# Kernel tuning notes

Hardware: AMD Instinct MI355X
Metric: run time of the kernel (lower is better)

The kernel has to match this reference:

```python
import math
import jax, jax.numpy as jnp
import numpy as np

B, N, D, O, S = 16, 4096, 64, 12, 32
K_TOD, K_DOW = 8, 4
M = K_TOD + K_DOW
A = 32  # attn_dim
ALPHA = 0.1
GATE_BOUND = 1.0
TEMP = 1.0


def setup_inputs() -> dict:
    key = jax.random.key(0)
    ks = jax.random.split(key, 10)
    sc = 0.05
    return {
        "H": jax.random.normal(ks[0], (B, N, D), jnp.float32),
        "ts_out": jax.random.uniform(ks[1], (B, O, 2), jnp.float32),
        "step_emb": jax.random.normal(ks[2], (B, O, S), jnp.float32),
        "key_emb": jax.random.normal(ks[3], (M, A), jnp.float32) * sc,
        "val_emb": jax.random.normal(ks[4], (M, D), jnp.float32) * sc,
        "Wk": jax.random.normal(ks[5], (A, 2), jnp.float32) * sc,
        "Wg": jax.random.normal(ks[6], (1, 2), jnp.float32) * sc,
        "bg": jnp.zeros((1,), jnp.float32),
        "Wq": jax.random.normal(ks[7], (A, D + S), jnp.float32) * sc,
        "bq": jnp.zeros((A,), jnp.float32),
    }


def _fourier_tokens(phase, K):
    # phase: [B,O]; returns [B,O,K,2] of (sin, cos) for harmonics k=1..K
    k = jnp.arange(1, K + 1, dtype=phase.dtype)  # [K]
    ang = 2.0 * math.pi * phase[..., None] * k   # [B,O,K]
    return jnp.stack([jnp.sin(ang), jnp.cos(ang)], axis=-1)


def reference(H, ts_out, step_emb, key_emb, val_emb, Wk, Wg, bg, Wq, bq):
    tod = ts_out[..., 0]
    dow = ts_out[..., 1]
    # Fourier time tokens: [B,O,M,2]
    tok = jnp.concatenate(
        [_fourier_tokens(tod, K_TOD), _fourier_tokens(dow, K_DOW)], axis=2
    )
    # keys / gates / values over the M tokens (tiny side)
    key = jnp.einsum("bomt,at->boma", tok, Wk) + key_emb[None, None]      # [B,O,M,A]
    gate = jnp.tanh(jnp.einsum("bomt,gt->bomg", tok, Wg) + bg) * GATE_BOUND  # [B,O,M,1]
    val = gate * val_emb[None, None]                                       # [B,O,M,D]
    # query: split Linear(D+S) into H-part and step-part to avoid materializing q_in
    qh = jnp.einsum("bnd,ad->bna", H, Wq[:, :D])            # [B,N,A]
    qs = jnp.einsum("bos,as->boa", step_emb, Wq[:, D:]) + bq  # [B,O,A]
    q = qh[:, None, :, :] + qs[:, :, None, :]                # [B,O,N,A]
    scale = 1.0 / (math.sqrt(float(A)) * max(TEMP, 1e-6))
    logits = jnp.einsum("bona,boma->bonm", q, key) * scale   # [B,O,N,M]
    attn = jax.nn.softmax(logits, axis=-1)
    delta = jnp.einsum("bonm,bomd->bond", attn, val)         # [B,O,N,D]
    H_time = H[:, None, :, :] + ALPHA * delta                # [B,O,N,D]
    return (H_time, attn, gate[..., 0])
```

## Files before the change

### kernel.cpp

```cpp
#include <hip/hip_runtime.h>
#include <math.h>

#define BB 16
#define NN 4096
#define DD 64
#define OO 12
#define SS 32
#define MM 12
#define AA 32

__global__ __launch_bounds__(256, 4) void stta_kernel(
    const float* __restrict__ H, const float* __restrict__ ts_out,
    const float* __restrict__ step_emb, const float* __restrict__ key_emb,
    const float* __restrict__ val_emb, const float* __restrict__ Wk,
    const float* __restrict__ Wg, const float* __restrict__ bgp,
    const float* __restrict__ Wq, const float* __restrict__ bq,
    float* __restrict__ out)
{
    const int b = blockIdx.y;
    const int n0 = blockIdx.x * 64;
    const int tid = threadIdx.x;

    __shared__ __align__(16) float s_wq[32 * 64];
    __shared__ __align__(16) float s_ke[MM * AA];
    __shared__ __align__(16) float s_ve[MM * DD];
    __shared__ __align__(16) float s_wk0[32];
    __shared__ __align__(16) float s_wk1[32];
    __shared__ __align__(16) float s_tokS[OO * MM];
    __shared__ __align__(16) float s_tokC[OO * MM];
    __shared__ __align__(16) float s_gate[OO * MM];
    __shared__ __align__(16) float s_qs[OO * AA];
    __shared__ __align__(16) float s_c2[OO * MM];

    float* outH    = out;
    float* outAttn = out + (size_t)BB * OO * NN * DD;
    float* outGate = outAttn + (size_t)BB * OO * NN * MM;

    const float scale = 0.17677669529663687f;

    {
        float4* dst = reinterpret_cast<float4*>(s_wq);
        for (int i = tid; i < 512; i += 256) {
            int a = i >> 4, dq = i & 15;
            dst[i] = reinterpret_cast<const float4*>(Wq + a * 96)[dq];
        }
    }
    {
        float4* dst = reinterpret_cast<float4*>(s_ke);
        const float4* src = reinterpret_cast<const float4*>(key_emb);
        for (int i = tid; i < (MM * AA) / 4; i += 256) dst[i] = src[i];
    }
    {
        float4* dst = reinterpret_cast<float4*>(s_ve);
        const float4* src = reinterpret_cast<const float4*>(val_emb);
        for (int i = tid; i < (MM * DD) / 4; i += 256) dst[i] = src[i];
    }
    if (tid < 32) { s_wk0[tid] = Wk[tid * 2]; s_wk1[tid] = Wk[tid * 2 + 1]; }

    const float wg0 = Wg[0], wg1 = Wg[1], bg0 = bgp[0];
    for (int i = tid; i < OO * MM; i += 256) {
        int o = i / MM, m = i - o * MM;
        float phase = ts_out[(b * OO + o) * 2 + (m < 8 ? 0 : 1)];
        float k = (m < 8) ? (float)(m + 1) : (float)(m - 7);
        float ang = 6.283185307179586f * phase * k;
        float sv = sinf(ang), cv = cosf(ang);
        s_tokS[i] = sv; s_tokC[i] = cv;
        float gv = tanhf(sv * wg0 + cv * wg1 + bg0);
        s_gate[i] = gv;
        if (blockIdx.x == 0) outGate[(b * OO + o) * MM + m] = gv;
    }
    for (int e = tid; e < OO * AA; e += 256) {
        int o = e >> 5, a = e & 31;
        float acc = bq[a];
        const float* se = step_emb + (b * OO + o) * SS;
        const float* wq = Wq + a * 96 + 64;
        #pragma unroll
        for (int s = 0; s < SS; s++) acc += se[s] * wq[s];
        s_qs[e] = acc;
    }
    __syncthreads();

    for (int i = tid; i < OO * MM; i += 256) {
        int o = i / MM, m = i - o * MM;
        float S = s_tokS[i], C = s_tokC[i];
        float acc = 0.f;
        const float* qs = s_qs + o * 32;
        const float* ke = s_ke + m * 32;
        #pragma unroll
        for (int a = 0; a < 32; a++)
            acc += qs[a] * (S * s_wk0[a] + C * s_wk1[a] + ke[a]);
        s_c2[i] = acc * scale;
    }
    __syncthreads();

    const int nl = tid >> 2, g = tid & 3;
    const int n = n0 + nl;

    const float4* hrow = reinterpret_cast<const float4*>(H + ((size_t)b * NN + n) * DD);
    float h[16];
    #pragma unroll
    for (int jj = 0; jj < 4; jj++) {
        float4 v = hrow[g + 4 * jj];
        h[jj*4+0] = v.x; h[jj*4+1] = v.y; h[jj*4+2] = v.z; h[jj*4+3] = v.w;
    }

    float uh = 0.f, vh = 0.f;
    float wh[12] = {0,0,0,0,0,0,0,0,0,0,0,0};
    {
        float qh[32];
        #pragma unroll
        for (int a = 0; a < 32; a++) {
            const float4* wq4 = reinterpret_cast<const float4*>(s_wq + a * 64);
            float acc = 0.f;
            #pragma unroll
            for (int jj = 0; jj < 4; jj++) {
                float4 w = wq4[g + 4 * jj];
                acc += h[jj*4+0]*w.x + h[jj*4+1]*w.y + h[jj*4+2]*w.z + h[jj*4+3]*w.w;
            }
            qh[a] = acc;
        }
        #pragma unroll
        for (int a = 0; a < 32; a++) qh[a] += __shfl_xor(qh[a], 1);
        #pragma unroll
        for (int a = 0; a < 32; a++) qh[a] += __shfl_xor(qh[a], 2);

        const float4* k0 = reinterpret_cast<const float4*>(s_wk0);
        const float4* k1 = reinterpret_cast<const float4*>(s_wk1);
        #pragma unroll
        for (int q = 0; q < 8; q++) {
            float4 a0 = k0[q], a1 = k1[q];
            uh += qh[q*4+0]*a0.x + qh[q*4+1]*a0.y + qh[q*4+2]*a0.z + qh[q*4+3]*a0.w;
            vh += qh[q*4+0]*a1.x + qh[q*4+1]*a1.y + qh[q*4+2]*a1.z + qh[q*4+3]*a1.w;
        }
        #pragma unroll
        for (int m = 0; m < 12; m++) {
            const float4* ke = reinterpret_cast<const float4*>(s_ke + m * 32);
            float acc = 0.f;
            #pragma unroll
            for (int q = 0; q < 8; q++) {
                float4 k4 = ke[q];
                acc += qh[q*4+0]*k4.x + qh[q*4+1]*k4.y + qh[q*4+2]*k4.z + qh[q*4+3]*k4.w;
            }
            wh[m] = acc * scale;
        }
        uh *= scale; vh *= scale;
    }

    const float4* ve4 = reinterpret_cast<const float4*>(s_ve);

    for (int op = 0; op < OO; op += 2) {
        const float4* tS  = reinterpret_cast<const float4*>(s_tokS + op * 12);
        const float4* tC  = reinterpret_cast<const float4*>(s_tokC + op * 12);
        const float4* tc2 = reinterpret_cast<const float4*>(s_c2   + op * 12);
        const float4* tgt = reinterpret_cast<const float4*>(s_gate + op * 12);

        float lg0[12], lg1[12];
        #pragma unroll
        for (int q = 0; q < 3; q++) {
            float4 S = tS[q], C = tC[q], c = tc2[q];
            lg0[q*4+0] = S.x*uh + C.x*vh + wh[q*4+0] + c.x;
            lg0[q*4+1] = S.y*uh + C.y*vh + wh[q*4+1] + c.y;
            lg0[q*4+2] = S.z*uh + C.z*vh + wh[q*4+2] + c.z;
            lg0[q*4+3] = S.w*uh + C.w*vh + wh[q*4+3] + c.w;
        }
        #pragma unroll
        for (int q = 0; q < 3; q++) {
            float4 S = tS[3+q], C = tC[3+q], c = tc2[3+q];
            lg1[q*4+0] = S.x*uh + C.x*vh + wh[q*4+0] + c.x;
            lg1[q*4+1] = S.y*uh + C.y*vh + wh[q*4+1] + c.y;
            lg1[q*4+2] = S.z*uh + C.z*vh + wh[q*4+2] + c.z;
            lg1[q*4+3] = S.w*uh + C.w*vh + wh[q*4+3] + c.w;
        }

        float mx0 = -1e30f, mx1 = -1e30f;
        #pragma unroll
        for (int m = 0; m < 12; m++) { mx0 = fmaxf(mx0, lg0[m]); mx1 = fmaxf(mx1, lg1[m]); }
        float sum0 = 0.f, sum1 = 0.f;
        #pragma unroll
        for (int m = 0; m < 12; m++) {
            lg0[m] = __expf(lg0[m] - mx0); sum0 += lg0[m];
            lg1[m] = __expf(lg1[m] - mx1); sum1 += lg1[m];
        }
        float inv0 = 1.f / sum0, inv1 = 1.f / sum1;
        #pragma unroll
        for (int m = 0; m < 12; m++) { lg0[m] *= inv0; lg1[m] *= inv1; }

        size_t abase0 = ((size_t)(b * OO + op) * NN + n) * MM;
        size_t abase1 = abase0 + (size_t)NN * MM;
        if (g == 0) {
            *reinterpret_cast<float4*>(outAttn + abase0) =
                make_float4(lg0[0], lg0[1], lg0[2], lg0[3]);
            *reinterpret_cast<float4*>(outAttn + abase1) =
                make_float4(lg1[0], lg1[1], lg1[2], lg1[3]);
        } else if (g == 1) {
            *reinterpret_cast<float4*>(outAttn + abase0 + 4) =
                make_float4(lg0[4], lg0[5], lg0[6], lg0[7]);
            *reinterpret_cast<float4*>(outAttn + abase1 + 4) =
                make_float4(lg1[4], lg1[5], lg1[6], lg1[7]);
        } else if (g == 2) {
            *reinterpret_cast<float4*>(outAttn + abase0 + 8) =
                make_float4(lg0[8], lg0[9], lg0[10], lg0[11]);
            *reinterpret_cast<float4*>(outAttn + abase1 + 8) =
                make_float4(lg1[8], lg1[9], lg1[10], lg1[11]);
        }

        #pragma unroll
        for (int q = 0; q < 3; q++) {
            float4 g0 = tgt[q], g1 = tgt[3+q];
            lg0[q*4+0] *= g0.x; lg0[q*4+1] *= g0.y; lg0[q*4+2] *= g0.z; lg0[q*4+3] *= g0.w;
            lg1[q*4+0] *= g1.x; lg1[q*4+1] *= g1.y; lg1[q*4+2] *= g1.z; lg1[q*4+3] *= g1.w;
        }

        size_t hbase = ((size_t)(b * OO + op) * NN + n) * DD;
        float4* outp0 = reinterpret_cast<float4*>(outH + hbase);
        float4* outp1 = reinterpret_cast<float4*>(outH + hbase + (size_t)NN * DD);
        #pragma unroll
        for (int jj = 0; jj < 4; jj++) {
            float ax0=0.f, ay0=0.f, az0=0.f, aw0=0.f;
            float ax1=0.f, ay1=0.f, az1=0.f, aw1=0.f;
            #pragma unroll
            for (int m = 0; m < 12; m++) {
                float4 vv = ve4[m * 16 + g + 4 * jj];
                ax0 += lg0[m]*vv.x; ay0 += lg0[m]*vv.y;
                az0 += lg0[m]*vv.z; aw0 += lg0[m]*vv.w;
                ax1 += lg1[m]*vv.x; ay1 += lg1[m]*vv.y;
                az1 += lg1[m]*vv.z; aw1 += lg1[m]*vv.w;
            }
            outp0[g + 4*jj] = make_float4(h[jj*4+0] + 0.1f*ax0, h[jj*4+1] + 0.1f*ay0,
                                          h[jj*4+2] + 0.1f*az0, h[jj*4+3] + 0.1f*aw0);
            outp1[g + 4*jj] = make_float4(h[jj*4+0] + 0.1f*ax1, h[jj*4+1] + 0.1f*ay1,
                                          h[jj*4+2] + 0.1f*az1, h[jj*4+3] + 0.1f*aw1);
        }
    }
}

extern "C" void kernel_launch(void* const* d_in, const int* in_sizes, int n_in,
                              void* d_out, int out_size, void* d_ws, size_t ws_size,
                              hipStream_t stream) {
    const float* H        = (const float*)d_in[0];
    const float* ts_out   = (const float*)d_in[1];
    const float* step_emb = (const float*)d_in[2];
    const float* key_emb  = (const float*)d_in[3];
    const float* val_emb  = (const float*)d_in[4];
    const float* Wk       = (const float*)d_in[5];
    const float* Wg       = (const float*)d_in[6];
    const float* bg       = (const float*)d_in[7];
    const float* Wq       = (const float*)d_in[8];
    const float* bq       = (const float*)d_in[9];
    float* outp = (float*)d_out;

    dim3 grid(NN / 64, BB);
    stta_kernel<<<grid, 256, 0, stream>>>(H, ts_out, step_emb, key_emb, val_emb,
                                          Wk, Wg, bg, Wq, bq, outp);
}
```

Baseline: 272.3 us.

## Fold Wq into key projections and process two rows per thread

Each block now precomputes a 14x64 matrix that folds Wq together with key_emb and Wk, so each row's logit terms come straight from H with 14 dot products instead of building a 32-wide query and then projecting it. Each thread also handles two rows (128 rows per block, half the grid), which spreads the block setup over more work and reuses the shared-memory loads. This raises register pressure, so launch bounds drop to 2 blocks per SM. The kernel is dominated by output writes, so the compute savings may matter little.

```diff
diff --git a/kernel.cpp b/kernel.cpp
--- a/kernel.cpp
+++ b/kernel.cpp
@@ -9,7 +9,29 @@
 #define MM 12
 #define AA 32
 
-__global__ __launch_bounds__(256, 4) void stta_kernel(
+__device__ __forceinline__ void softmax12(float* lg) {
+    float mx = -1e30f;
+    #pragma unroll
+    for (int m = 0; m < 12; m++) mx = fmaxf(mx, lg[m]);
+    float s = 0.f;
+    #pragma unroll
+    for (int m = 0; m < 12; m++) { lg[m] = __expf(lg[m] - mx); s += lg[m]; }
+    float inv = 1.f / s;
+    #pragma unroll
+    for (int m = 0; m < 12; m++) lg[m] *= inv;
+}
+
+__device__ __forceinline__ void attn_store(float* dst, const float* lg, int g) {
+    if (g == 0) {
+        *reinterpret_cast<float4*>(dst) = make_float4(lg[0], lg[1], lg[2], lg[3]);
+    } else if (g == 1) {
+        *reinterpret_cast<float4*>(dst + 4) = make_float4(lg[4], lg[5], lg[6], lg[7]);
+    } else if (g == 2) {
+        *reinterpret_cast<float4*>(dst + 8) = make_float4(lg[8], lg[9], lg[10], lg[11]);
+    }
+}
+
+__global__ __launch_bounds__(256, 2) void stta_kernel(
     const float* __restrict__ H, const float* __restrict__ ts_out,
     const float* __restrict__ step_emb, const float* __restrict__ key_emb,
     const float* __restrict__ val_emb, const float* __restrict__ Wk,
@@ -18,7 +40,7 @@
     float* __restrict__ out)
 {
     const int b = blockIdx.y;
-    const int n0 = blockIdx.x * 64;
+    const int n0 = blockIdx.x * 128;
     const int tid = threadIdx.x;
 
     __shared__ __align__(16) float s_wq[32 * 64];
@@ -31,6 +53,7 @@
     __shared__ __align__(16) float s_gate[OO * MM];
     __shared__ __align__(16) float s_qs[OO * AA];
     __shared__ __align__(16) float s_c2[OO * MM];
+    __shared__ __align__(16) float s_pm[14 * 64];
 
     float* outH    = out;
     float* outAttn = out + (size_t)BB * OO * NN * DD;
@@ -91,145 +114,135 @@
             acc += qs[a] * (S * s_wk0[a] + C * s_wk1[a] + ke[a]);
         s_c2[i] = acc * scale;
     }
+    for (int i = tid; i < 14 * 64; i += 256) {
+        int j = i >> 6, d = i & 63;
+        const float* coef = (j < 12) ? (s_ke + j * 32) : ((j == 12) ? s_wk0 : s_wk1);
+        float acc = 0.f;
+        #pragma unroll
+        for (int a = 0; a < 32; a++) acc += coef[a] * s_wq[a * 64 + d];
+        s_pm[i] = acc * scale;
+    }
     __syncthreads();
 
     const int nl = tid >> 2, g = tid & 3;
-    const int n = n0 + nl;
-
-    const float4* hrow = reinterpret_cast<const float4*>(H + ((size_t)b * NN + n) * DD);
-    float h[16];
+    const int r0 = n0 + nl;
+    const int r1 = r0 + 64;
+
+    const float4* hA = reinterpret_cast<const float4*>(H + ((size_t)b * NN + r0) * DD);
+    const float4* hB = reinterpret_cast<const float4*>(H + ((size_t)b * NN + r1) * DD);
+    float h0[16], h1[16];
     #pragma unroll
     for (int jj = 0; jj < 4; jj++) {
-        float4 v = hrow[g + 4 * jj];
-        h[jj*4+0] = v.x; h[jj*4+1] = v.y; h[jj*4+2] = v.z; h[jj*4+3] = v.w;
-    }
-
-    float uh = 0.f, vh = 0.f;
-    float wh[12] = {0,0,0,0,0,0,0,0,0,0,0,0};
-    {
-        float qh[32];
-        #pragma unroll
-        for (int a = 0; a < 32; a++) {
-            const float4* wq4 = reinterpret_cast<const float4*>(s_wq + a * 64);
-            float acc = 0.f;
-            #pragma unroll
-            for (int jj = 0; jj < 4; jj++) {
-                float4 w = wq4[g + 4 * jj];
-                acc += h[jj*4+0]*w.x + h[jj*4+1]*w.y + h[jj*4+2]*w.z + h[jj*4+3]*w.w;
-            }
-            qh[a] = acc;
-        }
-        #pragma unroll
-        for (int a = 0; a < 32; a++) qh[a] += __shfl_xor(qh[a], 1);
-        #pragma unroll
-        for (int a = 0; a < 32; a++) qh[a] += __shfl_xor(qh[a], 2);
-
-        const float4* k0 = reinterpret_cast<const float4*>(s_wk0);
-        const float4* k1 = reinterpret_cast<const float4*>(s_wk1);
-        #pragma unroll
-        for (int q = 0; q < 8; q++) {
-            float4 a0 = k0[q], a1 = k1[q];
-            uh += qh[q*4+0]*a0.x + qh[q*4+1]*a0.y + qh[q*4+2]*a0.z + qh[q*4+3]*a0.w;
-            vh += qh[q*4+0]*a1.x + qh[q*4+1]*a1.y + qh[q*4+2]*a1.z + qh[q*4+3]*a1.w;
-        }
-        #pragma unroll
-        for (int m = 0; m < 12; m++) {
-            const float4* ke = reinterpret_cast<const float4*>(s_ke + m * 32);
-            float acc = 0.f;
-            #pragma unroll
-            for (int q = 0; q < 8; q++) {
-                float4 k4 = ke[q];
-                acc += qh[q*4+0]*k4.x + qh[q*4+1]*k4.y + qh[q*4+2]*k4.z + qh[q*4+3]*k4.w;
-            }
-            wh[m] = acc * scale;
-        }
-        uh *= scale; vh *= scale;
-    }
+        float4 v0 = hA[g + 4 * jj];
+        float4 v1 = hB[g + 4 * jj];
+        h0[jj*4+0] = v0.x; h0[jj*4+1] = v0.y; h0[jj*4+2] = v0.z; h0[jj*4+3] = v0.w;
+        h1[jj*4+0] = v1.x; h1[jj*4+1] = v1.y; h1[jj*4+2] = v1.z; h1[jj*4+3] = v1.w;
+    }
+
+    float f0[14], f1[14];
+    #pragma unroll
+    for (int j = 0; j < 14; j++) {
+        const float4* pm = reinterpret_cast<const float4*>(s_pm + j * 64);
+        float a0 = 0.f, a1 = 0.f;
+        #pragma unroll
+        for (int jj = 0; jj < 4; jj++) {
+            float4 w = pm[g + 4 * jj];
+            a0 += h0[jj*4+0]*w.x + h0[jj*4+1]*w.y + h0[jj*4+2]*w.z + h0[jj*4+3]*w.w;
+            a1 += h1[jj*4+0]*w.x + h1[jj*4+1]*w.y + h1[jj*4+2]*w.z + h1[jj*4+3]*w.w;
+        }
+        f0[j] = a0; f1[j] = a1;
+    }
+    #pragma unroll
+    for (int j = 0; j < 14; j++) { f0[j] += __shfl_xor(f0[j], 1); f1[j] += __shfl_xor(f1[j], 1); }
+    #pragma unroll
+    for (int j = 0; j < 14; j++) { f0[j] += __shfl_xor(f0[j], 2); f1[j] += __shfl_xor(f1[j], 2); }
+
+    const float u0 = f0[12], v0c = f0[13];
+    const float u1 = f1[12], v1c = f1[13];
 
     const float4* ve4 = reinterpret_cast<const float4*>(s_ve);
 
+    #pragma unroll 1
     for (int op = 0; op < OO; op += 2) {
         const float4* tS  = reinterpret_cast<const float4*>(s_tokS + op * 12);
         const float4* tC  = reinterpret_cast<const float4*>(s_tokC + op * 12);
         const float4* tc2 = reinterpret_cast<const float4*>(s_c2   + op * 12);
         const float4* tgt = reinterpret_cast<const float4*>(s_gate + op * 12);
 
-        float lg0[12], lg1[12];
+        float lg00[12], lg01[12], lg10[12], lg11[12];
         #pragma unroll
         for (int q = 0; q < 3; q++) {
             float4 S = tS[q], C = tC[q], c = tc2[q];
-            lg0[q*4+0] = S.x*uh + C.x*vh + wh[q*4+0] + c.x;
-            lg0[q*4+1] = S.y*uh + C.y*vh + wh[q*4+1] + c.y;
-            lg0[q*4+2] = S.z*uh + C.z*vh + wh[q*4+2] + c.z;
-            lg0[q*4+3] = S.w*uh + C.w*vh + wh[q*4+3] + c.w;
+            lg00[q*4+0] = S.x*u0 + C.x*v0c + f0[q*4+0] + c.x;
+            lg00[q*4+1] = S.y*u0 + C.y*v0c + f0[q*4+1] + c.y;
+            lg00[q*4+2] = S.z*u0 + C.z*v0c + f0[q*4+2] + c.z;
+            lg00[q*4+3] = S.w*u0 + C.w*v0c + f0[q*4+3] + c.w;
+            lg10[q*4+0] = S.x*u1 + C.x*v1c + f1[q*4+0] + c.x;
+            lg10[q*4+1] = S.y*u1 + C.y*v1c + f1[q*4+1] + c.y;
+            lg10[q*4+2] = S.z*u1 + C.z*v1c + f1[q*4+2] + c.z;
+            lg10[q*4+3] = S.w*u1 + C.w*v1c + f1[q*4+3] + c.w;
         }
         #pragma unroll
         for (int q = 0; q < 3; q++) {
             float4 S = tS[3+q], C = tC[3+q], c = tc2[3+q];
-            lg1[q*4+0] = S.x*uh + C.x*vh + wh[q*4+0] + c.x;
-            lg1[q*4+1] = S.y*uh + C.y*vh + wh[q*4+1] + c.y;
-            lg1[q*4+2] = S.z*uh + C.z*vh + wh[q*4+2] + c.z;
-            lg1[q*4+3] = S.w*uh + C.w*vh + wh[q*4+3] + c.w;
-        }
-
-        float mx0 = -1e30f, mx1 = -1e30f;
-        #pragma unroll
-        for (int m = 0; m < 12; m++) { mx0 = fmaxf(mx0, lg0[m]); mx1 = fmaxf(mx1, lg1[m]); }
-        float sum0 = 0.f, sum1 = 0.f;
-        #pragma unroll
-        for (int m = 0; m < 12; m++) {
-            lg0[m] = __expf(lg0[m] - mx0); sum0 += lg0[m];
-            lg1[m] = __expf(lg1[m] - mx1); sum1 += lg1[m];
-        }
-        float inv0 = 1.f / sum0, inv1 = 1.f / sum1;
-        #pragma unroll
-        for (int m = 0; m < 12; m++) { lg0[m] *= inv0; lg1[m] *= inv1; }
-
-        size_t abase0 = ((size_t)(b * OO + op) * NN + n) * MM;
-        size_t abase1 = abase0 + (size_t)NN * MM;
-        if (g == 0) {
-            *reinterpret_cast<float4*>(outAttn + abase0) =
-                make_float4(lg0[0], lg0[1], lg0[2], lg0[3]);
-            *reinterpret_cast<float4*>(outAttn + abase1) =
-                make_float4(lg1[0], lg1[1], lg1[2], lg1[3]);
-        } else if (g == 1) {
-            *reinterpret_cast<float4*>(outAttn + abase0 + 4) =
-                make_float4(lg0[4], lg0[5], lg0[6], lg0[7]);
-            *reinterpret_cast<float4*>(outAttn + abase1 + 4) =
-                make_float4(lg1[4], lg1[5], lg1[6], lg1[7]);
-        } else if (g == 2) {
-            *reinterpret_cast<float4*>(outAttn + abase0 + 8) =
-                make_float4(lg0[8], lg0[9], lg0[10], lg0[11]);
-            *reinterpret_cast<float4*>(outAttn + abase1 + 8) =
-                make_float4(lg1[8], lg1[9], lg1[10], lg1[11]);
-        }
+            lg01[q*4+0] = S.x*u0 + C.x*v0c + f0[q*4+0] + c.x;
+            lg01[q*4+1] = S.y*u0 + C.y*v0c + f0[q*4+1] + c.y;
+            lg01[q*4+2] = S.z*u0 + C.z*v0c + f0[q*4+2] + c.z;
+            lg01[q*4+3] = S.w*u0 + C.w*v0c + f0[q*4+3] + c.w;
+            lg11[q*4+0] = S.x*u1 + C.x*v1c + f1[q*4+0] + c.x;
+            lg11[q*4+1] = S.y*u1 + C.y*v1c + f1[q*4+1] + c.y;
+            lg11[q*4+2] = S.z*u1 + C.z*v1c + f1[q*4+2] + c.z;
+            lg11[q*4+3] = S.w*u1 + C.w*v1c + f1[q*4+3] + c.w;
+        }
+
+        softmax12(lg00); softmax12(lg01); softmax12(lg10); softmax12(lg11);
+
+        size_t ab00 = ((size_t)(b * OO + op) * NN + r0) * MM;
+        size_t ab01 = ab00 + (size_t)NN * MM;
+        size_t ab10 = ab00 + (size_t)64 * MM;
+        size_t ab11 = ab10 + (size_t)NN * MM;
+        attn_store(outAttn + ab00, lg00, g);
+        attn_store(outAttn + ab01, lg01, g);
+        attn_store(outAttn + ab10, lg10, g);
+        attn_store(outAttn + ab11, lg11, g);
 
         #pragma unroll
         for (int q = 0; q < 3; q++) {
             float4 g0 = tgt[q], g1 = tgt[3+q];
-            lg0[q*4+0] *= g0.x; lg0[q*4+1] *= g0.y; lg0[q*4+2] *= g0.z; lg0[q*4+3] *= g0.w;
-            lg1[q*4+0] *= g1.x; lg1[q*4+1] *= g1.y; lg1[q*4+2] *= g1.z; lg1[q*4+3] *= g1.w;
-        }
-
-        size_t hbase = ((size_t)(b * OO + op) * NN + n) * DD;
-        float4* outp0 = reinterpret_cast<float4*>(outH + hbase);
-        float4* outp1 = reinterpret_cast<float4*>(outH + hbase + (size_t)NN * DD);
+            lg00[q*4+0] *= g0.x; lg00[q*4+1] *= g0.y; lg00[q*4+2] *= g0.z; lg00[q*4+3] *= g0.w;
+            lg10[q*4+0] *= g0.x; lg10[q*4+1] *= g0.y; lg10[q*4+2] *= g0.z; lg10[q*4+3] *= g0.w;
+            lg01[q*4+0] *= g1.x; lg01[q*4+1] *= g1.y; lg01[q*4+2] *= g1.z; lg01[q*4+3] *= g1.w;
+            lg11[q*4+0] *= g1.x; lg11[q*4+1] *= g1.y; lg11[q*4+2] *= g1.z; lg11[q*4+3] *= g1.w;
+        }
+
+        size_t hb00 = ((size_t)(b * OO + op) * NN + r0) * DD;
+        float4* o00 = reinterpret_cast<float4*>(outH + hb00);
+        float4* o01 = reinterpret_cast<float4*>(outH + hb00 + (size_t)NN * DD);
+        float4* o10 = reinterpret_cast<float4*>(outH + hb00 + (size_t)64 * DD);
+        float4* o11 = reinterpret_cast<float4*>(outH + hb00 + (size_t)NN * DD + (size_t)64 * DD);
         #pragma unroll
         for (int jj = 0; jj < 4; jj++) {
-            float ax0=0.f, ay0=0.f, az0=0.f, aw0=0.f;
-            float ax1=0.f, ay1=0.f, az1=0.f, aw1=0.f;
+            float4 a00 = make_float4(0.f,0.f,0.f,0.f);
+            float4 a01 = make_float4(0.f,0.f,0.f,0.f);
+            float4 a10 = make_float4(0.f,0.f,0.f,0.f);
+            float4 a11 = make_float4(0.f,0.f,0.f,0.f);
             #pragma unroll
             for (int m = 0; m < 12; m++) {
                 float4 vv = ve4[m * 16 + g + 4 * jj];
-                ax0 += lg0[m]*vv.x; ay0 += lg0[m]*vv.y;
-                az0 += lg0[m]*vv.z; aw0 += lg0[m]*vv.w;
-                ax1 += lg1[m]*vv.x; ay1 += lg1[m]*vv.y;
-                az1 += lg1[m]*vv.z; aw1 += lg1[m]*vv.w;
+                a00.x += lg00[m]*vv.x; a00.y += lg00[m]*vv.y; a00.z += lg00[m]*vv.z; a00.w += lg00[m]*vv.w;
+                a01.x += lg01[m]*vv.x; a01.y += lg01[m]*vv.y; a01.z += lg01[m]*vv.z; a01.w += lg01[m]*vv.w;
+                a10.x += lg10[m]*vv.x; a10.y += lg10[m]*vv.y; a10.z += lg10[m]*vv.z; a10.w += lg10[m]*vv.w;
+                a11.x += lg11[m]*vv.x; a11.y += lg11[m]*vv.y; a11.z += lg11[m]*vv.z; a11.w += lg11[m]*vv.w;
             }
-            outp0[g + 4*jj] = make_float4(h[jj*4+0] + 0.1f*ax0, h[jj*4+1] + 0.1f*ay0,
-                                          h[jj*4+2] + 0.1f*az0, h[jj*4+3] + 0.1f*aw0);
-            outp1[g + 4*jj] = make_float4(h[jj*4+0] + 0.1f*ax1, h[jj*4+1] + 0.1f*ay1,
-                                          h[jj*4+2] + 0.1f*az1, h[jj*4+3] + 0.1f*aw1);
+            int slot = g + 4 * jj;
+            o00[slot] = make_float4(h0[jj*4+0] + 0.1f*a00.x, h0[jj*4+1] + 0.1f*a00.y,
+                                    h0[jj*4+2] + 0.1f*a00.z, h0[jj*4+3] + 0.1f*a00.w);
+            o01[slot] = make_float4(h0[jj*4+0] + 0.1f*a01.x, h0[jj*4+1] + 0.1f*a01.y,
+                                    h0[jj*4+2] + 0.1f*a01.z, h0[jj*4+3] + 0.1f*a01.w);
+            o10[slot] = make_float4(h1[jj*4+0] + 0.1f*a10.x, h1[jj*4+1] + 0.1f*a10.y,
+                                    h1[jj*4+2] + 0.1f*a10.z, h1[jj*4+3] + 0.1f*a10.w);
+            o11[slot] = make_float4(h1[jj*4+0] + 0.1f*a11.x, h1[jj*4+1] + 0.1f*a11.y,
+                                    h1[jj*4+2] + 0.1f*a11.z, h1[jj*4+3] + 0.1f*a11.w);
         }
     }
 }
@@ -249,7 +262,7 @@
     const float* bq       = (const float*)d_in[9];
     float* outp = (float*)d_out;
 
-    dim3 grid(NN / 64, BB);
+    dim3 grid(NN / 128, BB);
     stta_kernel<<<grid, 256, 0, stream>>>(H, ts_out, step_emb, key_emb, val_emb,
                                           Wk, Wg, bg, Wq, bq, outp);
 }
```

Result: slower. 311.8 us (+14.5%).
